# Performance work log

Hardware: AMD Instinct MI355X
Metric: run time of the kernel (lower is better)

## Reference

```python
import jax, jax.numpy as jnp
import numpy as np

N = 50000
E = 800000
F_IN = 256
H = 64      # hidden_channels
NH = 4      # GAT heads

def setup_inputs() -> dict:
    key = jax.random.key(0)
    ks = jax.random.split(key, 16)
    x = jax.random.normal(ks[0], (N, F_IN), dtype=jnp.float32)
    edge_index = jax.random.randint(ks[1], (2, E), 0, N, dtype=jnp.int64)
    def w(k, shape, fan_in):
        return jax.random.normal(k, shape, dtype=jnp.float32) / np.sqrt(fan_in)
    return {
        "x": x, "edge_index": edge_index,
        "W1": w(ks[2], (F_IN, H), F_IN), "b1": jnp.zeros((H,), jnp.float32),
        "W2": w(ks[3], (H, H), H),       "b2": jnp.zeros((H,), jnp.float32),
        "Wg": w(ks[4], (H, NH * H), H),
        "att_src": w(ks[5], (NH, H), H), "att_dst": w(ks[6], (NH, H), H),
        "bg": jnp.zeros((NH * H,), jnp.float32),
        "Wf1": w(ks[7], (NH * H, H), NH * H), "bf1": jnp.zeros((H,), jnp.float32),
        "Wf2": w(ks[8], (H, 1), H),           "bf2": jnp.zeros((1,), jnp.float32),
    }

def _with_self_loops(edge_index):
    loops = jnp.arange(N, dtype=edge_index.dtype)
    src = jnp.concatenate([edge_index[0], loops])
    dst = jnp.concatenate([edge_index[1], loops])
    return src, dst

def _gcn(h, src, dst, W, b):
    # h: [N, d_in] -> [N, d_out]; symmetric norm D^-1/2 (A+I) D^-1/2
    h = h @ W
    deg = jax.ops.segment_sum(jnp.ones_like(dst, dtype=h.dtype), dst, num_segments=N)
    dinv = jnp.where(deg > 0, jax.lax.rsqrt(deg), 0.0)
    norm = dinv[src] * dinv[dst]                      # [E2]
    out = jax.ops.segment_sum(h[src] * norm[:, None], dst, num_segments=N)
    return out + b

def _gat(h, src, dst, Wg, att_src, att_dst, bg):
    hp = (h @ Wg).reshape(N, NH, H)                   # [N, NH, H]
    a_src = jnp.einsum('nhd,hd->nh', hp, att_src)     # [N, NH]
    a_dst = jnp.einsum('nhd,hd->nh', hp, att_dst)
    alpha = jax.nn.leaky_relu(a_src[src] + a_dst[dst], negative_slope=0.2)  # [E2, NH]
    amax = jax.ops.segment_max(alpha, dst, num_segments=N)
    e = jnp.exp(alpha - amax[dst])
    denom = jax.ops.segment_sum(e, dst, num_segments=N)
    coef = e / denom[dst]                             # [E2, NH]
    out = jax.ops.segment_sum(hp[src] * coef[:, :, None], dst, num_segments=N)
    return out.reshape(N, NH * H) + bg

def reference(x, edge_index, W1, b1, W2, b2, Wg, att_src, att_dst, bg, Wf1, bf1, Wf2, bf2):
    src, dst = _with_self_loops(edge_index)
    h = jax.nn.relu(_gcn(x, src, dst, W1, b1))        # dropout inactive (eval)
    h = jax.nn.relu(_gcn(h, src, dst, W2, b2))
    h = _gat(h, src, dst, Wg, att_src, att_dst, bg)
    h = jax.nn.relu(h @ Wf1 + bf1)
    return h @ Wf2 + bf2                              # [N, 1]
```

## Files before the change

### kernel.cpp

```cpp
#include <hip/hip_runtime.h>
#include <hip/hip_fp16.h>
#include <math.h>


#define CAP 64
#define CAPSH 6

typedef _Float16 v4h __attribute__((ext_vector_type(4)));
typedef float v4f __attribute__((ext_vector_type(4)));

__device__ __forceinline__ float lrelu02(float a) { return fmaxf(a, 0.2f * a); }

__device__ __forceinline__ float4 lrelu4(float4 a) {
    return make_float4(lrelu02(a.x), lrelu02(a.y), lrelu02(a.z), lrelu02(a.w));
}

__device__ __forceinline__ float4 exp4(float4 a) {
    return make_float4(__expf(a.x), __expf(a.y), __expf(a.z), __expf(a.w));
}

__device__ __forceinline__ float4 unpack4(float2 raw) {
    __half2 h01 = *(__half2*)&raw.x;
    __half2 h23 = *(__half2*)&raw.y;
    float2 f01 = __half22float2(h01);
    float2 f23 = __half22float2(h23);
    return make_float4(f01.x, f01.y, f23.x, f23.y);
}

__device__ __forceinline__ float2 pack4(float4 v) {
    float2 r;
    *(__half2*)&r.x = __float22half2_rn(make_float2(v.x, v.y));
    *(__half2*)&r.y = __float22half2_rn(make_float2(v.z, v.w));
    return r;
}


__launch_bounds__(256)
__global__ void k_scatter(const int* __restrict__ src, const int* __restrict__ dst, int E,
                          int* __restrict__ cnt, unsigned short* __restrict__ slots) {
    int tt = threadIdx.x;
    int base = blockIdx.x * 1024 + tt;
    int e0 = base, e1 = base + 256, e2 = base + 512, e3 = base + 768;
    int d0 = (e0 < E) ? dst[e0] : 0;
    int d1 = (e1 < E) ? dst[e1] : 0;
    int d2 = (e2 < E) ? dst[e2] : 0;
    int d3 = (e3 < E) ? dst[e3] : 0;
    int s0 = (e0 < E) ? src[e0] : 0;
    int s1 = (e1 < E) ? src[e1] : 0;
    int s2 = (e2 < E) ? src[e2] : 0;
    int s3 = (e3 < E) ? src[e3] : 0;
    int p0 = (e0 < E) ? atomicAdd(&cnt[d0], 1) : CAP;
    int p1 = (e1 < E) ? atomicAdd(&cnt[d1], 1) : CAP;
    int p2 = (e2 < E) ? atomicAdd(&cnt[d2], 1) : CAP;
    int p3 = (e3 < E) ? atomicAdd(&cnt[d3], 1) : CAP;
    if (p0 < CAP) slots[((size_t)d0 << CAPSH) + p0] = (unsigned short)s0;
    if (p1 < CAP) slots[((size_t)d1 << CAPSH) + p1] = (unsigned short)s1;
    if (p2 < CAP) slots[((size_t)d2 << CAPSH) + p2] = (unsigned short)s2;
    if (p3 < CAP) slots[((size_t)d3 << CAPSH) + p3] = (unsigned short)s3;
}


#define GEMM_BODY(BX, K, COLS)                                                     \
    __shared__ float As[16][68];                                                   \
    __shared__ float Bs[16][68];                                                   \
    const int row0 = (BX) * 64;                                                    \
    const int col0 = blockIdx.y * 64;                                              \
    const int t = threadIdx.x;                                                     \
    const int tx = t & 15;                                                         \
    const int ty = t >> 4;                                                         \
    const int lm = t >> 2;                                                         \
    const int lk4 = (t & 3) << 2;                                                  \
    const int wk = t >> 4;                                                         \
    const int wc = (t & 15) << 2;                                                  \
    float acc[4][4] = {};                                                          \
    for (int k0 = 0; k0 < K; k0 += 16) {                                           \
        float4 av = make_float4(0.f, 0.f, 0.f, 0.f);                               \
        int r = row0 + lm;                                                         \
        if (r < nrows) av = *(const float4*)(X + (size_t)r * K + k0 + lk4);        \
        As[lk4 + 0][lm] = av.x;                                                    \
        As[lk4 + 1][lm] = av.y;                                                    \
        As[lk4 + 2][lm] = av.z;                                                    \
        As[lk4 + 3][lm] = av.w;                                                    \
        *(float4*)&Bs[wk][wc] = *(const float4*)(W + (size_t)(k0 + wk) * COLS + col0 + wc); \
        __syncthreads();                                                           \
        _Pragma("unroll") for (int kk = 0; kk < 16; kk++) {                        \
            float4 a = *(const float4*)&As[kk][ty << 2];                           \
            float4 b = *(const float4*)&Bs[kk][tx << 2];                           \
            acc[0][0] = fmaf(a.x, b.x, acc[0][0]);                                 \
            acc[0][1] = fmaf(a.x, b.y, acc[0][1]);                                 \
            acc[0][2] = fmaf(a.x, b.z, acc[0][2]);                                 \
            acc[0][3] = fmaf(a.x, b.w, acc[0][3]);                                 \
            acc[1][0] = fmaf(a.y, b.x, acc[1][0]);                                 \
            acc[1][1] = fmaf(a.y, b.y, acc[1][1]);                                 \
            acc[1][2] = fmaf(a.y, b.z, acc[1][2]);                                 \
            acc[1][3] = fmaf(a.y, b.w, acc[1][3]);                                 \
            acc[2][0] = fmaf(a.z, b.x, acc[2][0]);                                 \
            acc[2][1] = fmaf(a.z, b.y, acc[2][1]);                                 \
            acc[2][2] = fmaf(a.z, b.z, acc[2][2]);                                 \
            acc[2][3] = fmaf(a.z, b.w, acc[2][3]);                                 \
            acc[3][0] = fmaf(a.w, b.x, acc[3][0]);                                 \
            acc[3][1] = fmaf(a.w, b.y, acc[3][1]);                                 \
            acc[3][2] = fmaf(a.w, b.z, acc[3][2]);                                 \
            acc[3][3] = fmaf(a.w, b.w, acc[3][3]);                                 \
        }                                                                          \
        __syncthreads();                                                           \
    }

__launch_bounds__(256)
__global__ void k_fused1(const int* __restrict__ cnt,
                         const float* __restrict__ X, const float* __restrict__ W,
                         __half* __restrict__ Y, int nrows, int gemmBlocks,
                         const float* __restrict__ Wg, const float* __restrict__ att_src,
                         const float* __restrict__ att_dst, const float* __restrict__ Wf1,
                         const float* __restrict__ bf1, const float* __restrict__ bg,
                         const float* __restrict__ W2, float* __restrict__ watt,
                         __half* __restrict__ WcF, __half* __restrict__ W2F,
                         float* __restrict__ bias2) {
    if ((int)blockIdx.x >= gemmBlocks) {
        int b2 = blockIdx.x - gemmBlocks;
        int tt = threadIdx.x;
        if (b2 < 64) {
            int idx = b2 * 256 + tt;
            int r = idx >> 6, c = idx & 63;
            int h = r >> 6, k = r & 63;
            float s = 0.f;
            for (int j = 0; j < 64; j++)
                s = fmaf(Wg[k * 256 + h * 64 + j], Wf1[(h * 64 + j) * 64 + c], s);
            int ks = r >> 4, kr = r & 15;
            int lfrag = ((kr >> 2) << 4) | (c & 15);
            int jf = kr & 3;
            int w = c >> 4;
            WcF[((((w << 4) | ks) << 6) | lfrag) * 4 + jf] = __float2half_rn(s);
        } else {
            for (int idx = tt; idx < 512; idx += 256) {
                int k = idx >> 3, c8 = idx & 7;
                int h = c8 & 3;
                const float* att = (c8 < 4) ? att_src : att_dst;
                float s = 0.f;
                for (int c = 0; c < 64; c++)
                    s = fmaf(Wg[k * 256 + h * 64 + c], att[h * 64 + c], s);
                watt[k * 8 + c8] = s;
            }
            if (tt < 64) {
                float s = bf1[tt];
                for (int j = 0; j < 256; j++) s = fmaf(bg[j], Wf1[j * 64 + tt], s);
                bias2[tt] = s;
            }
            for (int f = tt; f < 4096; f += 256) {
                int jf = f & 3, lfrag = (f >> 2) & 63, ws = f >> 8;
                int w = ws >> 2, ks = ws & 3;
                int k = ks * 16 + ((lfrag >> 4) << 2) + jf;
                int c = w * 16 + (lfrag & 15);
                W2F[f] = __float2half_rn(W2[k * 64 + c]);
            }
        }
        return;
    }
    GEMM_BODY(blockIdx.x, 256, 64)
#pragma unroll
    for (int i = 0; i < 4; i++) {
        int row = row0 + (ty << 2) + i;
        if (row >= nrows) break;
        float dv = rsqrtf((float)(min(cnt[row], CAP) + 1));
        float4 o = make_float4(acc[i][0] * dv, acc[i][1] * dv,
                               acc[i][2] * dv, acc[i][3] * dv);
        ((float2*)(Y + (size_t)row * 64))[tx] = pack4(o);
    }
}


__launch_bounds__(256)
__global__ void k_gcn1_gemm2(const __half* __restrict__ A, const unsigned short* __restrict__ slots,
                             const int* __restrict__ cnt, const float* __restrict__ b1,
                             const __half* __restrict__ W2F, __half* __restrict__ A2, int n) {
    __shared__ alignas(16) __half s_oh[16 * 68];
    __shared__ alignas(16) __half s_res[16 * 68];
    __shared__ float s_dv[16];
    int t = threadIdx.x;
    int lane = t & 63;
    int l = t & 15;
    int nb = t >> 4;
    int v = blockIdx.x * 16 + nb;
    bool act = (v < n);
    if (act) {
        int deg = min(cnt[v], CAP);
        const unsigned short* lst = slots + ((size_t)v << CAPSH);
        float dv = rsqrtf((float)(deg + 1));
        float4 a0 = unpack4(((const float2*)(A + (size_t)v * 64))[l]);
        float4 a1 = make_float4(0.f, 0.f, 0.f, 0.f);
        float4 a2 = a1, a3 = a1;
        int j = 0;
        for (; j + 7 < deg; j += 8) {
            ushort4 sa = *(const ushort4*)(lst + j);
            ushort4 sb = *(const ushort4*)(lst + j + 4);
            float4 t0 = unpack4(((const float2*)(A + (size_t)sa.x * 64))[l]);
            float4 t1 = unpack4(((const float2*)(A + (size_t)sa.y * 64))[l]);
            float4 t2 = unpack4(((const float2*)(A + (size_t)sa.z * 64))[l]);
            float4 t3 = unpack4(((const float2*)(A + (size_t)sa.w * 64))[l]);
            float4 t4 = unpack4(((const float2*)(A + (size_t)sb.x * 64))[l]);
            float4 t5 = unpack4(((const float2*)(A + (size_t)sb.y * 64))[l]);
            float4 t6 = unpack4(((const float2*)(A + (size_t)sb.z * 64))[l]);
            float4 t7 = unpack4(((const float2*)(A + (size_t)sb.w * 64))[l]);
            a0.x += t0.x + t4.x; a0.y += t0.y + t4.y; a0.z += t0.z + t4.z; a0.w += t0.w + t4.w;
            a1.x += t1.x + t5.x; a1.y += t1.y + t5.y; a1.z += t1.z + t5.z; a1.w += t1.w + t5.w;
            a2.x += t2.x + t6.x; a2.y += t2.y + t6.y; a2.z += t2.z + t6.z; a2.w += t2.w + t6.w;
            a3.x += t3.x + t7.x; a3.y += t3.y + t7.y; a3.z += t3.z + t7.z; a3.w += t3.w + t7.w;
        }
        for (; j + 3 < deg; j += 4) {
            ushort4 sa = *(const ushort4*)(lst + j);
            float4 t0 = unpack4(((const float2*)(A + (size_t)sa.x * 64))[l]);
            float4 t1 = unpack4(((const float2*)(A + (size_t)sa.y * 64))[l]);
            float4 t2 = unpack4(((const float2*)(A + (size_t)sa.z * 64))[l]);
            float4 t3 = unpack4(((const float2*)(A + (size_t)sa.w * 64))[l]);
            a0.x += t0.x; a0.y += t0.y; a0.z += t0.z; a0.w += t0.w;
            a1.x += t1.x; a1.y += t1.y; a1.z += t1.z; a1.w += t1.w;
            a2.x += t2.x; a2.y += t2.y; a2.z += t2.z; a2.w += t2.w;
            a3.x += t3.x; a3.y += t3.y; a3.z += t3.z; a3.w += t3.w;
        }
        for (; j < deg; j++) {
            float4 ta = unpack4(((const float2*)(A + (size_t)lst[j] * 64))[l]);
            a0.x += ta.x; a0.y += ta.y; a0.z += ta.z; a0.w += ta.w;
        }
        a0.x += a1.x + a2.x + a3.x;
        a0.y += a1.y + a2.y + a3.y;
        a0.z += a1.z + a2.z + a3.z;
        a0.w += a1.w + a2.w + a3.w;
        float4 b = ((const float4*)b1)[l];
        float4 o;
        o.x = fmaxf(fmaf(dv, a0.x, b.x), 0.f);
        o.y = fmaxf(fmaf(dv, a0.y, b.y), 0.f);
        o.z = fmaxf(fmaf(dv, a0.z, b.z), 0.f);
        o.w = fmaxf(fmaf(dv, a0.w, b.w), 0.f);
        *(float2*)&s_oh[nb * 68 + (l << 2)] = pack4(o);
        if (l == 0) s_dv[nb] = dv;
    } else {
        *(float2*)&s_oh[nb * 68 + (l << 2)] = make_float2(0.f, 0.f);
        if (l == 0) s_dv[nb] = 0.f;
    }
    __syncthreads();
    int w = t >> 6;
    v4f acc = {0.f, 0.f, 0.f, 0.f};
    int arow = (lane & 15) * 68;
    int acol = (lane >> 4) << 2;
#pragma unroll
    for (int ks = 0; ks < 4; ks++) {
        v4h a = *(const v4h*)&s_oh[arow + ks * 16 + acol];
        v4h bfr = *(const v4h*)&W2F[((((w << 2) | ks) << 6) | lane) << 2];
        acc = __builtin_amdgcn_mfma_f32_16x16x16f16(a, bfr, acc, 0, 0, 0);
    }
    int cc = (w << 4) | (lane & 15);
    int m0 = (lane >> 4) << 2;
#pragma unroll
    for (int j = 0; j < 4; j++)
        s_res[(m0 + j) * 68 + cc] = __float2half_rn(acc[j] * s_dv[m0 + j]);
    __syncthreads();
    if (act)
        ((float2*)(A2 + (size_t)v * 64))[l] = *(const float2*)&s_res[nb * 68 + (l << 2)];
}


__launch_bounds__(256)
__global__ void k_gcn2_att(const __half* __restrict__ T, const unsigned short* __restrict__ slots,
                           const int* __restrict__ cnt, const float* __restrict__ bias,
                           const float* __restrict__ watt, __half* __restrict__ Out,
                           float* __restrict__ asrc, float* __restrict__ adst, int n) {
    int t = threadIdx.x;
    int l = t & 15;
    int v = blockIdx.x * 16 + (t >> 4);
    if (v >= n) return;
    int deg = min(cnt[v], CAP);
    const unsigned short* lst = slots + ((size_t)v << CAPSH);
    float dv = rsqrtf((float)(deg + 1));
    float4 a0 = unpack4(((const float2*)(T + (size_t)v * 64))[l]);
    float4 a1 = make_float4(0.f, 0.f, 0.f, 0.f);
    float4 a2 = a1, a3 = a1;
    int j = 0;
    for (; j + 7 < deg; j += 8) {
        ushort4 sa = *(const ushort4*)(lst + j);
        ushort4 sb = *(const ushort4*)(lst + j + 4);
        float4 t0 = unpack4(((const float2*)(T + (size_t)sa.x * 64))[l]);
        float4 t1 = unpack4(((const float2*)(T + (size_t)sa.y * 64))[l]);
        float4 t2 = unpack4(((const float2*)(T + (size_t)sa.z * 64))[l]);
        float4 t3 = unpack4(((const float2*)(T + (size_t)sa.w * 64))[l]);
        float4 t4 = unpack4(((const float2*)(T + (size_t)sb.x * 64))[l]);
        float4 t5 = unpack4(((const float2*)(T + (size_t)sb.y * 64))[l]);
        float4 t6 = unpack4(((const float2*)(T + (size_t)sb.z * 64))[l]);
        float4 t7 = unpack4(((const float2*)(T + (size_t)sb.w * 64))[l]);
        a0.x += t0.x + t4.x; a0.y += t0.y + t4.y; a0.z += t0.z + t4.z; a0.w += t0.w + t4.w;
        a1.x += t1.x + t5.x; a1.y += t1.y + t5.y; a1.z += t1.z + t5.z; a1.w += t1.w + t5.w;
        a2.x += t2.x + t6.x; a2.y += t2.y + t6.y; a2.z += t2.z + t6.z; a2.w += t2.w + t6.w;
        a3.x += t3.x + t7.x; a3.y += t3.y + t7.y; a3.z += t3.z + t7.z; a3.w += t3.w + t7.w;
    }
    for (; j + 3 < deg; j += 4) {
        ushort4 sa = *(const ushort4*)(lst + j);
        float4 t0 = unpack4(((const float2*)(T + (size_t)sa.x * 64))[l]);
        float4 t1 = unpack4(((const float2*)(T + (size_t)sa.y * 64))[l]);
        float4 t2 = unpack4(((const float2*)(T + (size_t)sa.z * 64))[l]);
        float4 t3 = unpack4(((const float2*)(T + (size_t)sa.w * 64))[l]);
        a0.x += t0.x; a0.y += t0.y; a0.z += t0.z; a0.w += t0.w;
        a1.x += t1.x; a1.y += t1.y; a1.z += t1.z; a1.w += t1.w;
        a2.x += t2.x; a2.y += t2.y; a2.z += t2.z; a2.w += t2.w;
        a3.x += t3.x; a3.y += t3.y; a3.z += t3.z; a3.w += t3.w;
    }
    for (; j < deg; j++) {
        float4 ta = unpack4(((const float2*)(T + (size_t)lst[j] * 64))[l]);
        a0.x += ta.x; a0.y += ta.y; a0.z += ta.z; a0.w += ta.w;
    }
    a0.x += a1.x + a2.x + a3.x;
    a0.y += a1.y + a2.y + a3.y;
    a0.z += a1.z + a2.z + a3.z;
    a0.w += a1.w + a2.w + a3.w;
    float4 b = ((const float4*)bias)[l];
    float4 o;
    o.x = fmaxf(fmaf(dv, a0.x, b.x), 0.f);
    o.y = fmaxf(fmaf(dv, a0.y, b.y), 0.f);
    o.z = fmaxf(fmaf(dv, a0.z, b.z), 0.f);
    o.w = fmaxf(fmaf(dv, a0.w, b.w), 0.f);
    ((float2*)(Out + (size_t)v * 64))[l] = pack4(o);
    const float* wr = watt + (l << 2) * 8;
    float4 w0a = *(const float4*)(wr +  0), w0b = *(const float4*)(wr +  4);
    float4 w1a = *(const float4*)(wr +  8), w1b = *(const float4*)(wr + 12);
    float4 w2a = *(const float4*)(wr + 16), w2b = *(const float4*)(wr + 20);
    float4 w3a = *(const float4*)(wr + 24), w3b = *(const float4*)(wr + 28);
    float4 ds, dd;
    ds.x = o.x*w0a.x + o.y*w1a.x + o.z*w2a.x + o.w*w3a.x;
    ds.y = o.x*w0a.y + o.y*w1a.y + o.z*w2a.y + o.w*w3a.y;
    ds.z = o.x*w0a.z + o.y*w1a.z + o.z*w2a.z + o.w*w3a.z;
    ds.w = o.x*w0a.w + o.y*w1a.w + o.z*w2a.w + o.w*w3a.w;
    dd.x = o.x*w0b.x + o.y*w1b.x + o.z*w2b.x + o.w*w3b.x;
    dd.y = o.x*w0b.y + o.y*w1b.y + o.z*w2b.y + o.w*w3b.y;
    dd.z = o.x*w0b.z + o.y*w1b.z + o.z*w2b.z + o.w*w3b.z;
    dd.w = o.x*w0b.w + o.y*w1b.w + o.z*w2b.w + o.w*w3b.w;
    for (int off = 1; off <= 8; off <<= 1) {
        ds.x += __shfl_xor(ds.x, off); ds.y += __shfl_xor(ds.y, off);
        ds.z += __shfl_xor(ds.z, off); ds.w += __shfl_xor(ds.w, off);
        dd.x += __shfl_xor(dd.x, off); dd.y += __shfl_xor(dd.y, off);
        dd.z += __shfl_xor(dd.z, off); dd.w += __shfl_xor(dd.w, off);
    }
    if (l == 0) {
        ((float4*)asrc)[v] = ds;
        ((float4*)adst)[v] = dd;
    }
}


__launch_bounds__(256)
__global__ void k_gat_head(const __half* __restrict__ Bt, const unsigned short* __restrict__ slots,
                           const int* __restrict__ cnt, const float* __restrict__ asrc,
                           const float* __restrict__ adst, const __half* __restrict__ WcF,
                           const float* __restrict__ bias2, const float* __restrict__ Wf2,
                           const float* __restrict__ bf2, float* __restrict__ out, int n) {
    __shared__ alignas(16) __half s_aggh[16 * 260];
    __shared__ alignas(16) float s_e[16 * 68];
    __shared__ int s_sidx[16 * 17];
    __shared__ float s_part[16][4];
    int t = threadIdx.x;
    int lane = t & 63;
    int l = lane & 15;
    int nb = t >> 4;
    int v = blockIdx.x * 16 + nb;
    bool act = (v < n);
    if (act) {
        int deg = min(cnt[v], CAP);
        const unsigned short* lst = slots + ((size_t)v << CAPSH);
        float4 ad4 = ((const float4*)adst)[v];
        float4 as4 = ((const float4*)asrc)[v];
        float4 es = exp4(lrelu4(make_float4(as4.x + ad4.x, as4.y + ad4.y,
                                            as4.z + ad4.z, as4.w + ad4.w)));
        float4 esum = (l == 0) ? es : make_float4(0.f, 0.f, 0.f, 0.f);
        float4 bv = unpack4(((const float2*)(Bt + (size_t)v * 64))[l]);
        float4 acc0 = make_float4(es.x * bv.x, es.x * bv.y, es.x * bv.z, es.x * bv.w);
        float4 acc1 = make_float4(es.y * bv.x, es.y * bv.y, es.y * bv.z, es.y * bv.w);
        float4 acc2 = make_float4(es.z * bv.x, es.z * bv.y, es.z * bv.z, es.z * bv.w);
        float4 acc3 = make_float4(es.w * bv.x, es.w * bv.y, es.w * bv.z, es.w * bv.w);
        for (int c0 = 0; c0 < deg; c0 += 16) {
            int cl = min(16, deg - c0);
            float4 e = make_float4(0.f, 0.f, 0.f, 0.f);
            if (l < cl) {
                int s = lst[c0 + l];
                float4 sa = ((const float4*)asrc)[s];
                e = exp4(lrelu4(make_float4(sa.x + ad4.x, sa.y + ad4.y,
                                            sa.z + ad4.z, sa.w + ad4.w)));
                esum.x += e.x; esum.y += e.y; esum.z += e.z; esum.w += e.w;
                s_sidx[nb * 17 + l] = s;
            }
            *(float4*)&s_e[nb * 68 + (l << 2)] = e;
            __builtin_amdgcn_sched_barrier(0);
            for (int jj = 0; jj < cl; jj++) {
                int so = s_sidx[nb * 17 + jj];
                float4 ev = *(const float4*)&s_e[nb * 68 + (jj << 2)];
                float4 tv = unpack4(((const float2*)(Bt + (size_t)so * 64))[l]);
                acc0.x = fmaf(ev.x, tv.x, acc0.x); acc0.y = fmaf(ev.x, tv.y, acc0.y);
                acc0.z = fmaf(ev.x, tv.z, acc0.z); acc0.w = fmaf(ev.x, tv.w, acc0.w);
                acc1.x = fmaf(ev.y, tv.x, acc1.x); acc1.y = fmaf(ev.y, tv.y, acc1.y);
                acc1.z = fmaf(ev.y, tv.z, acc1.z); acc1.w = fmaf(ev.y, tv.w, acc1.w);
                acc2.x = fmaf(ev.z, tv.x, acc2.x); acc2.y = fmaf(ev.z, tv.y, acc2.y);
                acc2.z = fmaf(ev.z, tv.z, acc2.z); acc2.w = fmaf(ev.z, tv.w, acc2.w);
                acc3.x = fmaf(ev.w, tv.x, acc3.x); acc3.y = fmaf(ev.w, tv.y, acc3.y);
                acc3.z = fmaf(ev.w, tv.z, acc3.z); acc3.w = fmaf(ev.w, tv.w, acc3.w);
            }
        }
        for (int o = 8; o >= 1; o >>= 1) {
            esum.x += __shfl_xor(esum.x, o); esum.y += __shfl_xor(esum.y, o);
            esum.z += __shfl_xor(esum.z, o); esum.w += __shfl_xor(esum.w, o);
        }
        float i0 = 1.f / esum.x, i1 = 1.f / esum.y, i2 = 1.f / esum.z, i3 = 1.f / esum.w;
        *(float2*)&s_aggh[nb * 260 +   0 + (l << 2)] =
            pack4(make_float4(acc0.x*i0, acc0.y*i0, acc0.z*i0, acc0.w*i0));
        *(float2*)&s_aggh[nb * 260 +  64 + (l << 2)] =
            pack4(make_float4(acc1.x*i1, acc1.y*i1, acc1.z*i1, acc1.w*i1));
        *(float2*)&s_aggh[nb * 260 + 128 + (l << 2)] =
            pack4(make_float4(acc2.x*i2, acc2.y*i2, acc2.z*i2, acc2.w*i2));
        *(float2*)&s_aggh[nb * 260 + 192 + (l << 2)] =
            pack4(make_float4(acc3.x*i3, acc3.y*i3, acc3.z*i3, acc3.w*i3));
    } else {
        float2 z = make_float2(0.f, 0.f);
        *(float2*)&s_aggh[nb * 260 +   0 + (l << 2)] = z;
        *(float2*)&s_aggh[nb * 260 +  64 + (l << 2)] = z;
        *(float2*)&s_aggh[nb * 260 + 128 + (l << 2)] = z;
        *(float2*)&s_aggh[nb * 260 + 192 + (l << 2)] = z;
    }
    __syncthreads();
    int w = t >> 6;
    v4f accA = {0.f, 0.f, 0.f, 0.f};
    v4f accB = {0.f, 0.f, 0.f, 0.f};
    int arow = l * 260;
    int acol = (lane >> 4) << 2;
#pragma unroll
    for (int ks = 0; ks < 16; ks += 2) {
        v4h a0f = *(const v4h*)&s_aggh[arow + ks * 16 + acol];
        v4h b0f = *(const v4h*)&WcF[((((w << 4) | ks) << 6) | lane) << 2];
        accA = __builtin_amdgcn_mfma_f32_16x16x16f16(a0f, b0f, accA, 0, 0, 0);
        v4h a1f = *(const v4h*)&s_aggh[arow + (ks + 1) * 16 + acol];
        v4h b1f = *(const v4h*)&WcF[((((w << 4) | (ks + 1)) << 6) | lane) << 2];
        accB = __builtin_amdgcn_mfma_f32_16x16x16f16(a1f, b1f, accB, 0, 0, 0);
    }
    int cc = (w << 4) | l;
    float bb = bias2[cc], wq = Wf2[cc];
    float p0 = fmaxf(accA[0] + accB[0] + bb, 0.f) * wq;
    float p1 = fmaxf(accA[1] + accB[1] + bb, 0.f) * wq;
    float p2 = fmaxf(accA[2] + accB[2] + bb, 0.f) * wq;
    float p3 = fmaxf(accA[3] + accB[3] + bb, 0.f) * wq;
    for (int o = 1; o <= 8; o <<= 1) {
        p0 += __shfl_xor(p0, o); p1 += __shfl_xor(p1, o);
        p2 += __shfl_xor(p2, o); p3 += __shfl_xor(p3, o);
    }
    if (l == 0) {
        int m0 = (lane >> 4) << 2;
        s_part[m0 + 0][w] = p0; s_part[m0 + 1][w] = p1;
        s_part[m0 + 2][w] = p2; s_part[m0 + 3][w] = p3;
    }
    __syncthreads();
    if (t < 16 && blockIdx.x * 16 + t < n)
        out[blockIdx.x * 16 + t] =
            s_part[t][0] + s_part[t][1] + s_part[t][2] + s_part[t][3] + bf2[0];
}


extern "C" void kernel_launch(void* const* d_in, const int* in_sizes, int n_in,
                              void* d_out, int out_size, void* d_ws, size_t ws_size,
                              hipStream_t stream) {
    const float* x       = (const float*)d_in[0];
    const int*   ei      = (const int*)d_in[1];
    const float* W1      = (const float*)d_in[2];
    const float* b1      = (const float*)d_in[3];
    const float* W2      = (const float*)d_in[4];
    const float* b2      = (const float*)d_in[5];
    const float* Wg      = (const float*)d_in[6];
    const float* att_src = (const float*)d_in[7];
    const float* att_dst = (const float*)d_in[8];
    const float* bg      = (const float*)d_in[9];
    const float* Wf1     = (const float*)d_in[10];
    const float* bf1     = (const float*)d_in[11];
    const float* Wf2     = (const float*)d_in[12];
    const float* bf2     = (const float*)d_in[13];
    float* out = (float*)d_out;

    const int N = in_sizes[0] / 256;
    const int E = in_sizes[1] / 2;
    const int* src = ei;
    const int* dst = ei + E;

    char* p = (char*)d_ws;
    auto alloc = [&](size_t bytes) {
        void* r = (void*)p;
        p += (bytes + 255) & ~(size_t)255;
        return r;
    };
    __half* A   = (__half*)alloc((size_t)N * 64 * 2);
    __half* A2  = (__half*)alloc((size_t)N * 64 * 2);
    __half* B   = (__half*)alloc((size_t)N * 64 * 2);
    float* asrc = (float*)alloc((size_t)N * 4 * 4);
    float* adst = (float*)alloc((size_t)N * 4 * 4);
    int*   cnt  = (int*)alloc((size_t)N * 4);
    unsigned short* slots = (unsigned short*)alloc((size_t)N * CAP * 2);
    float* watt   = (float*)alloc(64 * 8 * 4);
    __half* WcF   = (__half*)alloc(256 * 64 * 2);
    __half* W2F   = (__half*)alloc(64 * 64 * 2);
    float* bias2  = (float*)alloc(64 * 4);

    const int gScat = (E + 1023) / 1024;
    const int grow = (N + 63) / 64;
    const int gagg = (N + 15) / 16;

    hipMemsetAsync(cnt, 0, (size_t)N * 4, stream);

    k_scatter<<<gScat, 256, 0, stream>>>(src, dst, E, cnt, slots);

    k_fused1<<<grow + 65, 256, 0, stream>>>(
        cnt, x, W1, A, N, grow,
        Wg, att_src, att_dst, Wf1, bf1, bg, W2, watt, WcF, W2F, bias2);

    k_gcn1_gemm2<<<gagg, 256, 0, stream>>>(A, slots, cnt, b1, W2F, A2, N);

    k_gcn2_att<<<gagg, 256, 0, stream>>>(A2, slots, cnt, b2, watt, B, asrc, adst, N);

    k_gat_head<<<gagg, 256, 0, stream>>>(B, slots, cnt, asrc, adst,
                                         WcF, bias2, Wf2, bf2, out, N);
}
```

Baseline: 264.1 us.

## Replace global-atomic edge scatter with two-pass bucketed scatter using shared-memory atomics

The single scatter kernel, which used a global atomic per edge on per-node counters, is replaced by two passes. The first pass bins edges into 256-node buckets using shared-memory histograms and one global atomic per bucket per block, staging packed (dst,src) pairs. The second pass has one block per bucket assign per-node slots with shared atomics and write counts directly, which also removes the memset of the node counters. It adds an extra staging write and read and an extra launch, and it drops edges once a bucket exceeds its fixed capacity.

```diff
diff --git a/kernel.cpp b/kernel.cpp
--- a/kernel.cpp
+++ b/kernel.cpp
@@ -5,6 +5,9 @@
 
 #define CAP 64
 #define CAPSH 6
+#define BSH 8
+#define NBKT 256
+#define BCAP 8192
 
 typedef _Float16 v4h __attribute__((ext_vector_type(4)));
 typedef float v4f __attribute__((ext_vector_type(4)));
@@ -36,27 +39,60 @@
 
 
 __launch_bounds__(256)
-__global__ void k_scatter(const int* __restrict__ src, const int* __restrict__ dst, int E,
-                          int* __restrict__ cnt, unsigned short* __restrict__ slots) {
-    int tt = threadIdx.x;
-    int base = blockIdx.x * 1024 + tt;
-    int e0 = base, e1 = base + 256, e2 = base + 512, e3 = base + 768;
-    int d0 = (e0 < E) ? dst[e0] : 0;
-    int d1 = (e1 < E) ? dst[e1] : 0;
-    int d2 = (e2 < E) ? dst[e2] : 0;
-    int d3 = (e3 < E) ? dst[e3] : 0;
-    int s0 = (e0 < E) ? src[e0] : 0;
-    int s1 = (e1 < E) ? src[e1] : 0;
-    int s2 = (e2 < E) ? src[e2] : 0;
-    int s3 = (e3 < E) ? src[e3] : 0;
-    int p0 = (e0 < E) ? atomicAdd(&cnt[d0], 1) : CAP;
-    int p1 = (e1 < E) ? atomicAdd(&cnt[d1], 1) : CAP;
-    int p2 = (e2 < E) ? atomicAdd(&cnt[d2], 1) : CAP;
-    int p3 = (e3 < E) ? atomicAdd(&cnt[d3], 1) : CAP;
-    if (p0 < CAP) slots[((size_t)d0 << CAPSH) + p0] = (unsigned short)s0;
-    if (p1 < CAP) slots[((size_t)d1 << CAPSH) + p1] = (unsigned short)s1;
-    if (p2 < CAP) slots[((size_t)d2 << CAPSH) + p2] = (unsigned short)s2;
-    if (p3 < CAP) slots[((size_t)d3 << CAPSH) + p3] = (unsigned short)s3;
+__global__ void k_bucket(const int* __restrict__ src, const int* __restrict__ dst, int E,
+                         int* __restrict__ bcnt, unsigned int* __restrict__ stage) {
+    __shared__ int hist[NBKT];
+    __shared__ int base[NBKT];
+    __shared__ int cur[NBKT];
+    int t = threadIdx.x;
+    hist[t] = 0; cur[t] = 0;
+    __syncthreads();
+    int base_e = blockIdx.x * 2048;
+    int d[8], s[8];
+#pragma unroll
+    for (int i = 0; i < 8; i++) {
+        int e = base_e + t + i * 256;
+        bool ok = (e < E);
+        d[i] = ok ? dst[e] : -1;
+        s[i] = ok ? src[e] : 0;
+        if (ok) atomicAdd(&hist[d[i] >> BSH], 1);
+    }
+    __syncthreads();
+    if (hist[t] > 0) base[t] = atomicAdd(&bcnt[t], hist[t]);
+    __syncthreads();
+#pragma unroll
+    for (int i = 0; i < 8; i++) {
+        if (d[i] >= 0) {
+            int b = d[i] >> BSH;
+            int p = base[b] + atomicAdd(&cur[b], 1);
+            if (p < BCAP)
+                stage[(size_t)b * BCAP + p] = ((unsigned)d[i] << 16) | (unsigned)s[i];
+        }
+    }
+}
+
+
+__launch_bounds__(256)
+__global__ void k_scatter2(const unsigned int* __restrict__ stage,
+                           const int* __restrict__ bcnt, int* __restrict__ cnt,
+                           unsigned short* __restrict__ slots, int n) {
+    __shared__ int lcnt[1 << BSH];
+    int t = threadIdx.x;
+    int k = blockIdx.x;
+    lcnt[t] = 0;
+    __syncthreads();
+    int ne = bcnt[k];
+    if (ne > BCAP) ne = BCAP;
+    const unsigned int* st = stage + (size_t)k * BCAP;
+    for (int i = t; i < ne; i += 256) {
+        unsigned int e = st[i];
+        int d = e >> 16;
+        int p = atomicAdd(&lcnt[d & ((1 << BSH) - 1)], 1);
+        if (p < CAP) slots[((size_t)d << CAPSH) + p] = (unsigned short)(e & 0xFFFF);
+    }
+    __syncthreads();
+    int v = (k << BSH) + t;
+    if (v < n) cnt[v] = lcnt[t];
 }
 
 
@@ -494,18 +530,23 @@
     float* adst = (float*)alloc((size_t)N * 4 * 4);
     int*   cnt  = (int*)alloc((size_t)N * 4);
     unsigned short* slots = (unsigned short*)alloc((size_t)N * CAP * 2);
+    int* bcnt = (int*)alloc(NBKT * 4);
+    unsigned int* stage = (unsigned int*)alloc((size_t)NBKT * BCAP * 4);
     float* watt   = (float*)alloc(64 * 8 * 4);
     __half* WcF   = (__half*)alloc(256 * 64 * 2);
     __half* W2F   = (__half*)alloc(64 * 64 * 2);
     float* bias2  = (float*)alloc(64 * 4);
 
-    const int gScat = (E + 1023) / 1024;
+    const int gBkt = (E + 2047) / 2048;
+    const int nbused = (N + (1 << BSH) - 1) >> BSH;
     const int grow = (N + 63) / 64;
     const int gagg = (N + 15) / 16;
 
-    hipMemsetAsync(cnt, 0, (size_t)N * 4, stream);
-
-    k_scatter<<<gScat, 256, 0, stream>>>(src, dst, E, cnt, slots);
+    hipMemsetAsync(bcnt, 0, NBKT * 4, stream);
+
+    k_bucket<<<gBkt, 256, 0, stream>>>(src, dst, E, bcnt, stage);
+
+    k_scatter2<<<nbused, 256, 0, stream>>>(stage, bcnt, cnt, slots, N);
 
     k_fused1<<<grow + 65, 256, 0, stream>>>(
         cnt, x, W1, A, N, grow,
```

Result: faster. 237.7 us (-10.0%).
